# Optimization experiments

Measured on AMD Instinct MI355X. Metric: run time of the kernel, lower is better.

## Reference

```python
import jax, jax.numpy as jnp
import numpy as np

B, N, D_MODEL, H, BLK = 2, 2048, 1024, 16, 128
TB = N // BLK  # 16 blocks per side
NEG = -1e30


def setup_inputs() -> dict:
    key = jax.random.key(0)
    kq, kk, kv, kb = jax.random.split(key, 4)
    q = jax.random.normal(kq, (B, N, D_MODEL), jnp.float32)
    k = jax.random.normal(kk, (B, N, D_MODEL), jnp.float32)
    v = jax.random.normal(kv, (B, N, D_MODEL), jnp.float32)
    tau = jnp.float32(1.0)
    mask = jnp.ones((B, 1, N, N), jnp.int32)
    block_sparse_mask = jax.random.randint(kb, (TB, TB), 0, 2).astype(jnp.int32)
    return {"q": q, "k": k, "v": v, "tau": tau, "mask": mask,
            "block_sparse_mask": block_sparse_mask}


def reference(q, k, v, tau, mask, block_sparse_mask):
    # Equivalent closed form of the tiled online-softmax loop (dropout p=0, eval
    # mode): processed blocks accumulate exactly masked softmax(tau*QK^T/sqrt(dk))@V;
    # rows whose every block is skipped keep O=0, l=0, m=-inf.
    Bq, Nq, D = q.shape
    d_k = D // H
    qh = q.reshape(Bq, Nq, H, d_k).transpose(0, 2, 1, 3)  # (B,H,N,dk)
    kh = k.reshape(Bq, Nq, H, d_k).transpose(0, 2, 1, 3)
    vh = v.reshape(Bq, Nq, H, d_k).transpose(0, 2, 1, 3)

    S = tau * jnp.einsum('bhqd,bhkd->bhqk', qh, kh) / np.sqrt(d_k).astype(np.float32)

    # expand block-sparse pattern to token resolution (N,N)
    bs = jnp.repeat(jnp.repeat(block_sparse_mask, BLK, axis=0), BLK, axis=1)
    allowed = (mask != 0) & (bs != 0)  # (B,1,N,N), broadcasts over heads

    S_m = jnp.where(allowed, S, NEG)
    m = jnp.max(S_m, axis=-1, keepdims=True)            # (B,H,N,1)
    P = jnp.exp(S_m - m) * allowed.astype(S.dtype)      # masked exp-weights
    l = jnp.sum(P, axis=-1, keepdims=True)              # (B,H,N,1)
    Ov = jnp.einsum('bhqk,bhkd->bhqd', P, vh)
    O = Ov / jnp.where(l > 0, l, 1.0)

    has_any = jnp.any(allowed, axis=-1, keepdims=True)  # (B,1,N,1)
    m_out = jnp.where(has_any, m, -jnp.inf)
    O_out = O.transpose(0, 2, 1, 3).reshape(Bq, Nq, D)
    return O_out, l, m_out
```

## Files before the change

### kernel.cpp

```cpp
#include <hip/hip_runtime.h>
#include <hip/hip_bf16.h>

#define B_   2
#define N_   2048
#define DM_  1024
#define H_   16
#define DK_  64
#define BLK_ 128
#define TB_  16

typedef unsigned short u16;
typedef unsigned int   u32;
using bf16x8 = __attribute__((ext_vector_type(8))) __bf16;
using f32x4  = __attribute__((ext_vector_type(4))) float;

#define KPAD 72
#define VPAD 136
#define PPAD 136
#define OPAD 68

__device__ __forceinline__ u32 pack_bf16(float a, float b) {
  __hip_bfloat162 h = __float22bfloat162_rn(make_float2(a, b));
  u32 u; __builtin_memcpy(&u, &h, 4); return u;
}
__device__ __forceinline__ bf16x8 pack8(float4 f0, float4 f1, float sc) {
  u32 w[4];
  w[0] = pack_bf16(f0.x * sc, f0.y * sc); w[1] = pack_bf16(f0.z * sc, f0.w * sc);
  w[2] = pack_bf16(f1.x * sc, f1.y * sc); w[3] = pack_bf16(f1.z * sc, f1.w * sc);
  bf16x8 r; __builtin_memcpy(&r, w, 16); return r;
}

__global__ void kv_convert(const float* __restrict__ k, const float* __restrict__ v,
                           u16* __restrict__ kb, u16* __restrict__ vt) {
  __shared__ u16 tile[BLK_][DK_ + 2];
  const int b = blockIdx.z, h = blockIdx.y, nb = blockIdx.x;
  const int t = threadIdx.x;
  const int rr = t >> 4, cc = (t & 15) * 4;
  {
    const float* kg = k + ((size_t)(b * N_ + nb * BLK_)) * DM_ + h * DK_;
    u16* kd = kb + ((size_t)((b * H_ + h) * N_) + nb * BLK_) * DK_;
#pragma unroll
    for (int i = 0; i < 8; ++i) {
      const int r = rr + i * 16;
      const float4 f = *(const float4*)(kg + (size_t)r * DM_ + cc);
      *(uint2*)(kd + r * DK_ + cc) = make_uint2(pack_bf16(f.x, f.y), pack_bf16(f.z, f.w));
    }
  }
  {
    const float* vg = v + ((size_t)(b * N_ + nb * BLK_)) * DM_ + h * DK_;
#pragma unroll
    for (int i = 0; i < 8; ++i) {
      const int r = rr + i * 16;
      const float4 f = *(const float4*)(vg + (size_t)r * DM_ + cc);
      *(u32*)(&tile[r][cc])     = pack_bf16(f.x, f.y);
      *(u32*)(&tile[r][cc + 2]) = pack_bf16(f.z, f.w);
    }
    __syncthreads();
    const int d = t & 63, n0 = (t >> 6) * 32;
    u16* og = vt + ((size_t)(b * H_ + h) * DK_ + d) * N_ + nb * BLK_ + n0;
#pragma unroll
    for (int j = 0; j < 32; j += 8) {
      u16 tmp[8];
#pragma unroll
      for (int x = 0; x < 8; ++x) tmp[x] = tile[n0 + j + x][d];
      uint4 w; __builtin_memcpy(&w, tmp, 16);
      *(uint4*)(og + j) = w;
    }
  }
}

__global__ void mask_flags_kernel(const int* __restrict__ mask, const int* __restrict__ bs,
                                  int* __restrict__ flags) {
  const int blk = blockIdx.x;
  const int kb = blk % TB_, qb = (blk / TB_) % TB_, b = blk / (TB_ * TB_);
  const int t = threadIdx.x;
  const int* mg = mask + (size_t)b * N_ * N_ + (size_t)(qb * BLK_) * N_ + kb * BLK_;
  int all1 = 1, any1 = 0;
  for (int i = t; i < BLK_ * BLK_ / 4; i += 256) {
    const int r = i >> 5, c = (i & 31) * 4;
    const int4 mv = *(const int4*)(mg + (size_t)r * N_ + c);
    all1 &= (mv.x != 0) & (mv.y != 0) & (mv.z != 0) & (mv.w != 0);
    any1 |= (mv.x != 0) | (mv.y != 0) | (mv.z != 0) | (mv.w != 0);
  }
  __shared__ int sAll[4], sAny[4];
  const int wv = t >> 6;
  const int wAll = __all(all1), wAny = __any(any1);
  if ((t & 63) == 0) { sAll[wv] = wAll; sAny[wv] = wAny; }
  __syncthreads();
  if (t == 0) {
    const int A = sAll[0] & sAll[1] & sAll[2] & sAll[3];
    const int O = sAny[0] | sAny[1] | sAny[2] | sAny[3];
    int f = 0;
    if (bs[qb * TB_ + kb] != 0 && O) f = A ? 1 : 2;
    flags[blk] = f;
  }
}

__global__ __launch_bounds__(256, 2)
void attn_kernel(const float* __restrict__ q_, const u16* __restrict__ kb_,
                 const u16* __restrict__ vt, const float* __restrict__ tau_p,
                 const int* __restrict__ mask, const int* __restrict__ flags,
                 float* __restrict__ o_out, float* __restrict__ l_out,
                 float* __restrict__ m_out) {
  __shared__ __align__(16) u16 lds[BLK_ * KPAD + DK_ * VPAD + BLK_ * PPAD];
  u16* Ks  = lds;
  u16* Vts = Ks + BLK_ * KPAD;
  u16* Ps  = Vts + DK_ * VPAD;
  float* Os = (float*)lds;

  const int idx = blockIdx.x;
  const int bh = idx & 31, qb128 = idx >> 5;
  const int b = bh >> 4, h = bh & 15;
  const int t = threadIdx.x;
  const int wave = t >> 6, lane = t & 63, quad = lane >> 4, col = lane & 15;

  const int* flg = flags + (b * TB_ + qb128) * TB_;
  u32 actmask = 0, mixmask = 0;
#pragma unroll
  for (int i = 0; i < TB_; ++i) {
    const int f = flg[i];
    actmask |= (f != 0) ? (1u << i) : 0u;
    mixmask |= (f == 2) ? (1u << i) : 0u;
  }

  int qg[2];
  qg[0] = qb128 * BLK_ + wave * 32 + col;
  qg[1] = qg[0] + 16;

  const float qscale = tau_p[0] * 0.125f * 1.44269504f;
  bf16x8 bq[2][2];
#pragma unroll
  for (int nt = 0; nt < 2; ++nt) {
    const float* qr = q_ + ((size_t)(b * N_ + qg[nt])) * DM_ + h * DK_;
#pragma unroll
    for (int half = 0; half < 2; ++half) {
      const float4 f0 = *(const float4*)(qr + half * 32 + quad * 8);
      const float4 f1 = *(const float4*)(qr + half * 32 + quad * 8 + 4);
      bq[nt][half] = pack8(f0, f1, qscale);
    }
  }

  float m_run[2]  = {-INFINITY, -INFINITY};
  float m_true[2] = {-INFINITY, -INFINITY};
  float l_run[2] = {0.f, 0.f};
  f32x4 oacc[2][4];
#pragma unroll
  for (int nt = 0; nt < 2; ++nt)
#pragma unroll
    for (int mt = 0; mt < 4; ++mt) oacc[nt][mt] = (f32x4){0.f, 0.f, 0.f, 0.f};

  const u16* kbase = kb_ + (size_t)(b * H_ + h) * N_ * DK_;
  const u16* vbase = vt + (size_t)(b * H_ + h) * DK_ * N_;

  u32 rem = actmask;
  while (rem) {
    const int cur = (int)__builtin_ctz(rem);
    rem &= rem - 1;
    const int mix = (mixmask >> cur) & 1;

    __syncthreads();
    {
      const u16* ks = kbase + (size_t)cur * BLK_ * DK_;
      const u16* vs = vbase + cur * BLK_;
      uint4 kr[4], vr[4];
#pragma unroll
      for (int j = 0; j < 4; ++j) {
        const int i = t + 256 * j;
        kr[j] = *(const uint4*)(ks + i * 8);
        vr[j] = *(const uint4*)(vs + (size_t)(i >> 4) * N_ + (i & 15) * 8);
      }
#pragma unroll
      for (int j = 0; j < 4; ++j) {
        const int i = t + 256 * j;
        *(uint4*)(Ks + (i >> 3) * KPAD + (i & 7) * 8) = kr[j];
        *(uint4*)(Vts + (i >> 4) * VPAD + (i & 15) * 8) = vr[j];
      }
    }
    __syncthreads();

#pragma unroll
    for (int nt = 0; nt < 2; ++nt) {
      f32x4 st[8];
      __builtin_amdgcn_s_setprio(1);
#pragma unroll
      for (int kt = 0; kt < 8; ++kt) {
        const bf16x8 a0 = *(const bf16x8*)(Ks + (kt * 16 + col) * KPAD + quad * 8);
        const bf16x8 a1 = *(const bf16x8*)(Ks + (kt * 16 + col) * KPAD + 32 + quad * 8);
        f32x4 c = (f32x4){0.f, 0.f, 0.f, 0.f};
        c = __builtin_amdgcn_mfma_f32_16x16x32_bf16(a0, bq[nt][0], c, 0, 0, 0);
        c = __builtin_amdgcn_mfma_f32_16x16x32_bf16(a1, bq[nt][1], c, 0, 0, 0);
        st[kt] = c;
      }
      __builtin_amdgcn_s_setprio(0);
      if (mix) {
        const int* mg = mask + (size_t)b * N_ * N_ + (size_t)qg[nt] * N_ + cur * BLK_;
#pragma unroll
        for (int kt = 0; kt < 8; ++kt) {
          const int4 mv = *(const int4*)(mg + kt * 16 + quad * 4);
          if (!mv.x) st[kt][0] = -1e30f;
          if (!mv.y) st[kt][1] = -1e30f;
          if (!mv.z) st[kt][2] = -1e30f;
          if (!mv.w) st[kt][3] = -1e30f;
        }
      }
      float mx = -INFINITY;
#pragma unroll
      for (int kt = 0; kt < 8; ++kt)
        mx = fmaxf(mx, fmaxf(fmaxf(st[kt][0], st[kt][1]), fmaxf(st[kt][2], st[kt][3])));
      mx = fmaxf(mx, __shfl_xor(mx, 16, 64));
      mx = fmaxf(mx, __shfl_xor(mx, 32, 64));
      m_true[nt] = fmaxf(m_true[nt], mx);

      const float mold = m_run[nt];
      float mnew = mold;
      if (!__all(mx <= mold + 8.f)) {
        mnew = fmaxf(mold, mx);
        const float alpha = __builtin_amdgcn_exp2f(mold - mnew);
        l_run[nt] *= alpha;
#pragma unroll
        for (int mt = 0; mt < 4; ++mt)
#pragma unroll
          for (int r = 0; r < 4; ++r) oacc[nt][mt][r] *= alpha;
        m_run[nt] = mnew;
      }

      const int qloc = wave * 32 + nt * 16 + col;
      float s = 0.f;
      if (!mix) {
#pragma unroll
        for (int kt = 0; kt < 8; ++kt) {
          const float p0 = __builtin_amdgcn_exp2f(st[kt][0] - mnew);
          const float p1 = __builtin_amdgcn_exp2f(st[kt][1] - mnew);
          const float p2 = __builtin_amdgcn_exp2f(st[kt][2] - mnew);
          const float p3 = __builtin_amdgcn_exp2f(st[kt][3] - mnew);
          s += (p0 + p1) + (p2 + p3);
          *(uint2*)(Ps + qloc * PPAD + kt * 16 + quad * 4) =
              make_uint2(pack_bf16(p0, p1), pack_bf16(p2, p3));
        }
      } else {
#pragma unroll
        for (int kt = 0; kt < 8; ++kt) {
          const float p0 = st[kt][0] <= -1e29f ? 0.f : __builtin_amdgcn_exp2f(st[kt][0] - mnew);
          const float p1 = st[kt][1] <= -1e29f ? 0.f : __builtin_amdgcn_exp2f(st[kt][1] - mnew);
          const float p2 = st[kt][2] <= -1e29f ? 0.f : __builtin_amdgcn_exp2f(st[kt][2] - mnew);
          const float p3 = st[kt][3] <= -1e29f ? 0.f : __builtin_amdgcn_exp2f(st[kt][3] - mnew);
          s += (p0 + p1) + (p2 + p3);
          *(uint2*)(Ps + qloc * PPAD + kt * 16 + quad * 4) =
              make_uint2(pack_bf16(p0, p1), pack_bf16(p2, p3));
        }
      }
      s += __shfl_xor(s, 16, 64);
      s += __shfl_xor(s, 32, 64);
      l_run[nt] += s;
    }

    __builtin_amdgcn_s_setprio(1);
#pragma unroll
    for (int ks = 0; ks < 4; ++ks) {
      bf16x8 bfrag[2];
#pragma unroll
      for (int nt = 0; nt < 2; ++nt)
        bfrag[nt] = *(const bf16x8*)(Ps + (wave * 32 + nt * 16 + col) * PPAD + ks * 32 + quad * 8);
#pragma unroll
      for (int mt = 0; mt < 4; ++mt) {
        const bf16x8 av = *(const bf16x8*)(Vts + (mt * 16 + col) * VPAD + ks * 32 + quad * 8);
#pragma unroll
        for (int nt = 0; nt < 2; ++nt)
          oacc[nt][mt] = __builtin_amdgcn_mfma_f32_16x16x32_bf16(av, bfrag[nt], oacc[nt][mt], 0, 0, 0);
      }
    }
    __builtin_amdgcn_s_setprio(0);
  }

  __syncthreads();
#pragma unroll
  for (int nt = 0; nt < 2; ++nt) {
    const float inv = l_run[nt] > 0.f ? 1.f / l_run[nt] : 1.f;
    const int qloc = wave * 32 + nt * 16 + col;
#pragma unroll
    for (int mt = 0; mt < 4; ++mt) {
      float4 w = make_float4(oacc[nt][mt][0] * inv, oacc[nt][mt][1] * inv,
                             oacc[nt][mt][2] * inv, oacc[nt][mt][3] * inv);
      *(float4*)(Os + qloc * OPAD + mt * 16 + quad * 4) = w;
    }
  }
  __syncthreads();
  float* ob = o_out + ((size_t)(b * N_ + qb128 * BLK_)) * DM_ + h * DK_;
#pragma unroll
  for (int j = 0; j < 8; ++j) {
    const int i = t + 256 * j;
    const int r = i >> 4, c4 = (i & 15) * 4;
    const float4 w = *(const float4*)(Os + r * OPAD + c4);
    *(float4*)(ob + (size_t)r * DM_ + c4) = w;
  }
  if (quad == 0) {
#pragma unroll
    for (int nt = 0; nt < 2; ++nt) {
      const size_t oi = (size_t)(b * H_ + h) * N_ + qg[nt];
      const float lv = l_run[nt] > 0.f
          ? l_run[nt] * __builtin_amdgcn_exp2f(m_run[nt] - m_true[nt]) : 0.f;
      l_out[oi] = lv;
      m_out[oi] = l_run[nt] > 0.f ? m_true[nt] * 0.69314718056f : -INFINITY;
    }
  }
}

extern "C" void kernel_launch(void* const* d_in, const int* in_sizes, int n_in,
                              void* d_out, int out_size, void* d_ws, size_t ws_size,
                              hipStream_t stream) {
  const float* q   = (const float*)d_in[0];
  const float* k   = (const float*)d_in[1];
  const float* v   = (const float*)d_in[2];
  const float* tau = (const float*)d_in[3];
  const int* mask  = (const int*)d_in[4];
  const int* bs    = (const int*)d_in[5];
  float* out = (float*)d_out;

  const size_t plane = (size_t)B_ * H_ * N_ * DK_;
  u16* kb = (u16*)d_ws;
  u16* vt = kb + plane;
  int* flags = (int*)(vt + plane);

  kv_convert<<<dim3(N_ / BLK_, H_, B_), 256, 0, stream>>>(k, v, kb, vt);
  mask_flags_kernel<<<B_ * TB_ * TB_, 256, 0, stream>>>(mask, bs, flags);

  float* o_out = out;
  float* l_out = out + (size_t)B_ * N_ * DM_;
  float* m_out = l_out + (size_t)B_ * H_ * N_;
  attn_kernel<<<dim3(TB_ * 32), 256, 0, stream>>>(q, kb, vt, tau, mask, flags,
                                                  o_out, l_out, m_out);
}
```

Before: 165.7 us.

## Halve query rows per attention block to double grid size and occupancy

Each workgroup now handles 64 query rows (16 per wave) instead of 128, doubling the grid to 1024 blocks and shrinking the P buffer in LDS. Launch bounds rise to 3 blocks per SIMD-group so more waves can hide latency. The cost is that every K/V tile is loaded from global memory and staged into LDS twice as often, halving reuse per load, and each wave issues fewer MFMAs per barrier.

```diff
diff --git a/kernel.cpp b/kernel.cpp
--- a/kernel.cpp
+++ b/kernel.cpp
@@ -18,6 +18,7 @@
 #define VPAD 136
 #define PPAD 136
 #define OPAD 68
+#define QROWS 64
 
 __device__ __forceinline__ u32 pack_bf16(float a, float b) {
   __hip_bfloat162 h = __float22bfloat162_rn(make_float2(a, b));
@@ -96,21 +97,22 @@
   }
 }
 
-__global__ __launch_bounds__(256, 2)
+__global__ __launch_bounds__(256, 3)
 void attn_kernel(const float* __restrict__ q_, const u16* __restrict__ kb_,
                  const u16* __restrict__ vt, const float* __restrict__ tau_p,
                  const int* __restrict__ mask, const int* __restrict__ flags,
                  float* __restrict__ o_out, float* __restrict__ l_out,
                  float* __restrict__ m_out) {
-  __shared__ __align__(16) u16 lds[BLK_ * KPAD + DK_ * VPAD + BLK_ * PPAD];
+  __shared__ __align__(16) u16 lds[BLK_ * KPAD + DK_ * VPAD + QROWS * PPAD];
   u16* Ks  = lds;
   u16* Vts = Ks + BLK_ * KPAD;
   u16* Ps  = Vts + DK_ * VPAD;
   float* Os = (float*)lds;
 
   const int idx = blockIdx.x;
-  const int bh = idx & 31, qb128 = idx >> 5;
+  const int bh = idx & 31, qb64 = idx >> 5;
   const int b = bh >> 4, h = bh & 15;
+  const int qb128 = qb64 >> 1;
   const int t = threadIdx.x;
   const int wave = t >> 6, lane = t & 63, quad = lane >> 4, col = lane & 15;
 
@@ -123,31 +125,26 @@
     mixmask |= (f == 2) ? (1u << i) : 0u;
   }
 
-  int qg[2];
-  qg[0] = qb128 * BLK_ + wave * 32 + col;
-  qg[1] = qg[0] + 16;
+  const int qg = qb64 * QROWS + wave * 16 + col;
 
   const float qscale = tau_p[0] * 0.125f * 1.44269504f;
-  bf16x8 bq[2][2];
-#pragma unroll
-  for (int nt = 0; nt < 2; ++nt) {
-    const float* qr = q_ + ((size_t)(b * N_ + qg[nt])) * DM_ + h * DK_;
+  bf16x8 bq[2];
+  {
+    const float* qr = q_ + ((size_t)(b * N_ + qg)) * DM_ + h * DK_;
 #pragma unroll
     for (int half = 0; half < 2; ++half) {
       const float4 f0 = *(const float4*)(qr + half * 32 + quad * 8);
       const float4 f1 = *(const float4*)(qr + half * 32 + quad * 8 + 4);
-      bq[nt][half] = pack8(f0, f1, qscale);
-    }
-  }
-
-  float m_run[2]  = {-INFINITY, -INFINITY};
-  float m_true[2] = {-INFINITY, -INFINITY};
-  float l_run[2] = {0.f, 0.f};
-  f32x4 oacc[2][4];
-#pragma unroll
-  for (int nt = 0; nt < 2; ++nt)
-#pragma unroll
-    for (int mt = 0; mt < 4; ++mt) oacc[nt][mt] = (f32x4){0.f, 0.f, 0.f, 0.f};
+      bq[half] = pack8(f0, f1, qscale);
+    }
+  }
+
+  float m_run  = -INFINITY;
+  float m_true = -INFINITY;
+  float l_run  = 0.f;
+  f32x4 oacc[4];
+#pragma unroll
+  for (int mt = 0; mt < 4; ++mt) oacc[mt] = (f32x4){0.f, 0.f, 0.f, 0.f};
 
   const u16* kbase = kb_ + (size_t)(b * H_ + h) * N_ * DK_;
   const u16* vbase = vt + (size_t)(b * H_ + h) * DK_ * N_;
@@ -178,130 +175,118 @@
     }
     __syncthreads();
 
-#pragma unroll
-    for (int nt = 0; nt < 2; ++nt) {
-      f32x4 st[8];
-      __builtin_amdgcn_s_setprio(1);
+    f32x4 st[8];
+    __builtin_amdgcn_s_setprio(1);
+#pragma unroll
+    for (int kt = 0; kt < 8; ++kt) {
+      const bf16x8 a0 = *(const bf16x8*)(Ks + (kt * 16 + col) * KPAD + quad * 8);
+      const bf16x8 a1 = *(const bf16x8*)(Ks + (kt * 16 + col) * KPAD + 32 + quad * 8);
+      f32x4 c = (f32x4){0.f, 0.f, 0.f, 0.f};
+      c = __builtin_amdgcn_mfma_f32_16x16x32_bf16(a0, bq[0], c, 0, 0, 0);
+      c = __builtin_amdgcn_mfma_f32_16x16x32_bf16(a1, bq[1], c, 0, 0, 0);
+      st[kt] = c;
+    }
+    __builtin_amdgcn_s_setprio(0);
+    if (mix) {
+      const int* mg = mask + (size_t)b * N_ * N_ + (size_t)qg * N_ + cur * BLK_;
 #pragma unroll
       for (int kt = 0; kt < 8; ++kt) {
-        const bf16x8 a0 = *(const bf16x8*)(Ks + (kt * 16 + col) * KPAD + quad * 8);
-        const bf16x8 a1 = *(const bf16x8*)(Ks + (kt * 16 + col) * KPAD + 32 + quad * 8);
-        f32x4 c = (f32x4){0.f, 0.f, 0.f, 0.f};
-        c = __builtin_amdgcn_mfma_f32_16x16x32_bf16(a0, bq[nt][0], c, 0, 0, 0);
-        c = __builtin_amdgcn_mfma_f32_16x16x32_bf16(a1, bq[nt][1], c, 0, 0, 0);
-        st[kt] = c;
-      }
-      __builtin_amdgcn_s_setprio(0);
-      if (mix) {
-        const int* mg = mask + (size_t)b * N_ * N_ + (size_t)qg[nt] * N_ + cur * BLK_;
-#pragma unroll
-        for (int kt = 0; kt < 8; ++kt) {
-          const int4 mv = *(const int4*)(mg + kt * 16 + quad * 4);
-          if (!mv.x) st[kt][0] = -1e30f;
-          if (!mv.y) st[kt][1] = -1e30f;
-          if (!mv.z) st[kt][2] = -1e30f;
-          if (!mv.w) st[kt][3] = -1e30f;
-        }
-      }
-      float mx = -INFINITY;
-#pragma unroll
-      for (int kt = 0; kt < 8; ++kt)
-        mx = fmaxf(mx, fmaxf(fmaxf(st[kt][0], st[kt][1]), fmaxf(st[kt][2], st[kt][3])));
-      mx = fmaxf(mx, __shfl_xor(mx, 16, 64));
-      mx = fmaxf(mx, __shfl_xor(mx, 32, 64));
-      m_true[nt] = fmaxf(m_true[nt], mx);
-
-      const float mold = m_run[nt];
-      float mnew = mold;
-      if (!__all(mx <= mold + 8.f)) {
-        mnew = fmaxf(mold, mx);
-        const float alpha = __builtin_amdgcn_exp2f(mold - mnew);
-        l_run[nt] *= alpha;
-#pragma unroll
-        for (int mt = 0; mt < 4; ++mt)
-#pragma unroll
-          for (int r = 0; r < 4; ++r) oacc[nt][mt][r] *= alpha;
-        m_run[nt] = mnew;
-      }
-
-      const int qloc = wave * 32 + nt * 16 + col;
-      float s = 0.f;
-      if (!mix) {
-#pragma unroll
-        for (int kt = 0; kt < 8; ++kt) {
-          const float p0 = __builtin_amdgcn_exp2f(st[kt][0] - mnew);
-          const float p1 = __builtin_amdgcn_exp2f(st[kt][1] - mnew);
-          const float p2 = __builtin_amdgcn_exp2f(st[kt][2] - mnew);
-          const float p3 = __builtin_amdgcn_exp2f(st[kt][3] - mnew);
-          s += (p0 + p1) + (p2 + p3);
-          *(uint2*)(Ps + qloc * PPAD + kt * 16 + quad * 4) =
-              make_uint2(pack_bf16(p0, p1), pack_bf16(p2, p3));
-        }
-      } else {
-#pragma unroll
-        for (int kt = 0; kt < 8; ++kt) {
-          const float p0 = st[kt][0] <= -1e29f ? 0.f : __builtin_amdgcn_exp2f(st[kt][0] - mnew);
-          const float p1 = st[kt][1] <= -1e29f ? 0.f : __builtin_amdgcn_exp2f(st[kt][1] - mnew);
-          const float p2 = st[kt][2] <= -1e29f ? 0.f : __builtin_amdgcn_exp2f(st[kt][2] - mnew);
-          const float p3 = st[kt][3] <= -1e29f ? 0.f : __builtin_amdgcn_exp2f(st[kt][3] - mnew);
-          s += (p0 + p1) + (p2 + p3);
-          *(uint2*)(Ps + qloc * PPAD + kt * 16 + quad * 4) =
-              make_uint2(pack_bf16(p0, p1), pack_bf16(p2, p3));
-        }
-      }
-      s += __shfl_xor(s, 16, 64);
-      s += __shfl_xor(s, 32, 64);
-      l_run[nt] += s;
-    }
+        const int4 mv = *(const int4*)(mg + kt * 16 + quad * 4);
+        if (!mv.x) st[kt][0] = -1e30f;
+        if (!mv.y) st[kt][1] = -1e30f;
+        if (!mv.z) st[kt][2] = -1e30f;
+        if (!mv.w) st[kt][3] = -1e30f;
+      }
+    }
+    float mx = -INFINITY;
+#pragma unroll
+    for (int kt = 0; kt < 8; ++kt)
+      mx = fmaxf(mx, fmaxf(fmaxf(st[kt][0], st[kt][1]), fmaxf(st[kt][2], st[kt][3])));
+    mx = fmaxf(mx, __shfl_xor(mx, 16, 64));
+    mx = fmaxf(mx, __shfl_xor(mx, 32, 64));
+    m_true = fmaxf(m_true, mx);
+
+    const float mold = m_run;
+    float mnew = mold;
+    if (!__all(mx <= mold + 8.f)) {
+      mnew = fmaxf(mold, mx);
+      const float alpha = __builtin_amdgcn_exp2f(mold - mnew);
+      l_run *= alpha;
+#pragma unroll
+      for (int mt = 0; mt < 4; ++mt)
+#pragma unroll
+        for (int r = 0; r < 4; ++r) oacc[mt][r] *= alpha;
+      m_run = mnew;
+    }
+
+    const int qloc = wave * 16 + col;
+    float s = 0.f;
+    if (!mix) {
+#pragma unroll
+      for (int kt = 0; kt < 8; ++kt) {
+        const float p0 = __builtin_amdgcn_exp2f(st[kt][0] - mnew);
+        const float p1 = __builtin_amdgcn_exp2f(st[kt][1] - mnew);
+        const float p2 = __builtin_amdgcn_exp2f(st[kt][2] - mnew);
+        const float p3 = __builtin_amdgcn_exp2f(st[kt][3] - mnew);
+        s += (p0 + p1) + (p2 + p3);
+        *(uint2*)(Ps + qloc * PPAD + kt * 16 + quad * 4) =
+            make_uint2(pack_bf16(p0, p1), pack_bf16(p2, p3));
+      }
+    } else {
+#pragma unroll
+      for (int kt = 0; kt < 8; ++kt) {
+        const float p0 = st[kt][0] <= -1e29f ? 0.f : __builtin_amdgcn_exp2f(st[kt][0] - mnew);
+        const float p1 = st[kt][1] <= -1e29f ? 0.f : __builtin_amdgcn_exp2f(st[kt][1] - mnew);
+        const float p2 = st[kt][2] <= -1e29f ? 0.f : __builtin_amdgcn_exp2f(st[kt][2] - mnew);
+        const float p3 = st[kt][3] <= -1e29f ? 0.f : __builtin_amdgcn_exp2f(st[kt][3] - mnew);
+        s += (p0 + p1) + (p2 + p3);
+        *(uint2*)(Ps + qloc * PPAD + kt * 16 + quad * 4) =
+            make_uint2(pack_bf16(p0, p1), pack_bf16(p2, p3));
+      }
+    }
+    s += __shfl_xor(s, 16, 64);
+    s += __shfl_xor(s, 32, 64);
+    l_run += s;
 
     __builtin_amdgcn_s_setprio(1);
 #pragma unroll
     for (int ks = 0; ks < 4; ++ks) {
-      bf16x8 bfrag[2];
-#pragma unroll
-      for (int nt = 0; nt < 2; ++nt)
-        bfrag[nt] = *(const bf16x8*)(Ps + (wave * 32 + nt * 16 + col) * PPAD + ks * 32 + quad * 8);
+      const bf16x8 bfrag = *(const bf16x8*)(Ps + qloc * PPAD + ks * 32 + quad * 8);
 #pragma unroll
       for (int mt = 0; mt < 4; ++mt) {
         const bf16x8 av = *(const bf16x8*)(Vts + (mt * 16 + col) * VPAD + ks * 32 + quad * 8);
-#pragma unroll
-        for (int nt = 0; nt < 2; ++nt)
-          oacc[nt][mt] = __builtin_amdgcn_mfma_f32_16x16x32_bf16(av, bfrag[nt], oacc[nt][mt], 0, 0, 0);
+        oacc[mt] = __builtin_amdgcn_mfma_f32_16x16x32_bf16(av, bfrag, oacc[mt], 0, 0, 0);
       }
     }
     __builtin_amdgcn_s_setprio(0);
   }
 
   __syncthreads();
-#pragma unroll
-  for (int nt = 0; nt < 2; ++nt) {
-    const float inv = l_run[nt] > 0.f ? 1.f / l_run[nt] : 1.f;
-    const int qloc = wave * 32 + nt * 16 + col;
+  {
+    const float inv = l_run > 0.f ? 1.f / l_run : 1.f;
+    const int qloc = wave * 16 + col;
 #pragma unroll
     for (int mt = 0; mt < 4; ++mt) {
-      float4 w = make_float4(oacc[nt][mt][0] * inv, oacc[nt][mt][1] * inv,
-                             oacc[nt][mt][2] * inv, oacc[nt][mt][3] * inv);
+      float4 w = make_float4(oacc[mt][0] * inv, oacc[mt][1] * inv,
+                             oacc[mt][2] * inv, oacc[mt][3] * inv);
       *(float4*)(Os + qloc * OPAD + mt * 16 + quad * 4) = w;
     }
   }
   __syncthreads();
-  float* ob = o_out + ((size_t)(b * N_ + qb128 * BLK_)) * DM_ + h * DK_;
-#pragma unroll
-  for (int j = 0; j < 8; ++j) {
+  float* ob = o_out + ((size_t)(b * N_ + qb64 * QROWS)) * DM_ + h * DK_;
+#pragma unroll
+  for (int j = 0; j < 4; ++j) {
     const int i = t + 256 * j;
     const int r = i >> 4, c4 = (i & 15) * 4;
     const float4 w = *(const float4*)(Os + r * OPAD + c4);
     *(float4*)(ob + (size_t)r * DM_ + c4) = w;
   }
   if (quad == 0) {
-#pragma unroll
-    for (int nt = 0; nt < 2; ++nt) {
-      const size_t oi = (size_t)(b * H_ + h) * N_ + qg[nt];
-      const float lv = l_run[nt] > 0.f
-          ? l_run[nt] * __builtin_amdgcn_exp2f(m_run[nt] - m_true[nt]) : 0.f;
-      l_out[oi] = lv;
-      m_out[oi] = l_run[nt] > 0.f ? m_true[nt] * 0.69314718056f : -INFINITY;
-    }
+    const size_t oi = (size_t)(b * H_ + h) * N_ + qg;
+    const float lv = l_run > 0.f
+        ? l_run * __builtin_amdgcn_exp2f(m_run - m_true) : 0.f;
+    l_out[oi] = lv;
+    m_out[oi] = l_run > 0.f ? m_true * 0.69314718056f : -INFINITY;
   }
 }
 
@@ -327,6 +312,6 @@
   float* o_out = out;
   float* l_out = out + (size_t)B_ * N_ * DM_;
   float* m_out = l_out + (size_t)B_ * H_ * N_;
-  attn_kernel<<<dim3(TB_ * 32), 256, 0, stream>>>(q, kb, vt, tau, mask, flags,
-                                                  o_out, l_out, m_out);
-}
+  attn_kernel<<<dim3((N_ / QROWS) * 32), 256, 0, stream>>>(q, kb, vt, tau, mask, flags,
+                                                           o_out, l_out, m_out);
+}
```

Result: no change. 167.2 us (+0.9%).
